# Performance work log

Measured on AMD Instinct MI355X. Metric: run time of the kernel, lower is better.

The kernel has to match this reference:

```python
import jax, jax.numpy as jnp
import numpy as np


def setup_inputs() -> dict:
    key = jax.random.key(0)
    k1, k2, k3 = jax.random.split(key, 3)
    N, Ci, H, W = 16, 64, 224, 224
    Co, K = 128, 3
    x = jax.random.normal(k1, (N, Ci, H, W), dtype=jnp.float32)
    # Kaiming-like scale for conv weight
    conv_weight = jax.random.normal(k2, (Co, Ci, K, K), dtype=jnp.float32) * (1.0 / np.sqrt(Ci * K * K))
    conv_bias = jax.random.normal(k3, (Co,), dtype=jnp.float32) * 0.01
    return {"x": x, "conv_weight": conv_weight, "conv_bias": conv_bias}


def reference(x, conv_weight, conv_bias):
    # conv2d, stride=1, padding=0 (VALID), NCHW / OIHW
    y = jax.lax.conv_general_dilated(
        x, conv_weight,
        window_strides=(1, 1),
        padding="VALID",
        dimension_numbers=("NCHW", "OIHW", "NCHW"),
    ) + conv_bias[None, :, None, None]  # [N, Co, OH, OW]
    # min over output channels (keepdim), then double tanh
    m = jnp.min(y, axis=1, keepdims=True)  # [N, 1, OH, OW]
    return jnp.tanh(jnp.tanh(m))
```

## Files before the change

### kernel.cpp

```cpp
#include <hip/hip_runtime.h>
#include <hip/hip_bf16.h>
#include <math.h>

#define NN   16
#define CI   64
#define HH   224
#define WW   224
#define CO   128
#define OHH  222
#define OWW  222

#define WS_NEED (36*4*64*16)

typedef short  short8  __attribute__((ext_vector_type(8)));
typedef float  f32x16  __attribute__((ext_vector_type(16)));
typedef float  f32x4   __attribute__((ext_vector_type(4)));

__device__ static inline unsigned f2bf_pk(float a, float b) {
  __hip_bfloat162 h = __float22bfloat162_rn(make_float2(a, b));
  return *reinterpret_cast<unsigned*>(&h);
}

__global__ __launch_bounds__(256) void prep_w_kernel(const float* __restrict__ wt,
                                                     unsigned char* __restrict__ ws) {
  int t    = blockIdx.x * 256 + threadIdx.x;
  int lane = t & 63;
  int f    = t >> 6;
  int s    = f >> 2;
  int ct   = f & 3;
  int tap  = s >> 2;
  int cic  = s & 3;
  int kh   = tap / 3, kw = tap % 3;
  int co   = ct * 32 + (lane & 31);
  int k0   = cic * 16 + (lane >> 5) * 8;
  unsigned pk[4];
#pragma unroll
  for (int j = 0; j < 4; ++j) {
    int ci0 = k0 + 2 * j;
    float a = wt[(size_t)co * 576 + (ci0    ) * 9 + kh * 3 + kw];
    float b = wt[(size_t)co * 576 + (ci0 + 1) * 9 + kh * 3 + kw];
    pk[j] = f2bf_pk(a, b);
  }
  ((uint4*)ws)[t] = make_uint4(pk[0], pk[1], pk[2], pk[3]);
}

__global__ __launch_bounds__(512, 4) void conv_min_kernel(
    const float* __restrict__ x, const float* __restrict__ bias,
    const unsigned char* __restrict__ ws, float* __restrict__ out) {
  __shared__ __align__(16) unsigned char smem[10 * 34 * 128];

  int bid = blockIdx.x;
  bid = (bid & 7) * (NN * 28 * 7 / 8) + (bid >> 3);

  int owt  = bid % 7;
  int rest = bid / 7;
  int oht  = rest % 28;
  int n    = rest / 28;
  int ow0  = (owt < 6) ? owt * 32 : 190;
  int oh0  = oht * 8;

  int tid   = threadIdx.x;
  int wv    = tid >> 6;
  int lane  = tid & 63;
  int mg    = wv >> 1;
  int ng    = wv & 1;
  int mrow  = lane & 31;
  int khalf = lane >> 5;

  const short8* wf = (const short8*)ws;
  int bbase = ng * 128 + lane;
  short8 bb[3][2];
#pragma unroll
  for (int ct = 0; ct < 2; ++ct) bb[0][ct] = wf[0 * 256 + ct * 64 + bbase];
#pragma unroll
  for (int ct = 0; ct < 2; ++ct) bb[1][ct] = wf[1 * 256 + ct * 64 + bbase];

  {
    int colm = (tid & 15) * 2;
    int q    = tid >> 4;
    const float* xb = x + (size_t)n * 64 * 50176;
#pragma unroll 1
    for (int r = 0; r < 10; ++r) {
      int rg = oh0 + r; if (rg > 223) rg = 223;
      const float* xr = xb + (size_t)rg * 224;
      {
        int ci = q * 2;
        const float* s0 = xr + (size_t)ci * 50176 + ow0 + colm;
        float2 a2 = *(const float2*)s0;
        float2 b2 = *(const float2*)(s0 + 50176);
        unsigned u0 = f2bf_pk(a2.x, b2.x);
        unsigned u1 = f2bf_pk(a2.y, b2.y);
        int cc = q >> 2, jw = (q & 3) * 4;
        *(unsigned*)(smem + (r * 34 + colm    ) * 128 + (((cc + colm    ) & 7) << 4) + jw) = u0;
        *(unsigned*)(smem + (r * 34 + colm + 1) * 128 + (((cc + colm + 1) & 7) << 4) + jw) = u1;
      }
      if (tid < 64) {
        int cole = 32 + (tid & 1);
        int ppe  = tid >> 1;
        const float* s0 = xr + (size_t)(ppe * 2) * 50176 + ow0 + cole;
        float a = s0[0], b = s0[50176];
        *(unsigned*)(smem + (r * 34 + cole) * 128 + ((((ppe >> 2) + cole) & 7) << 4) + (ppe & 3) * 4) =
            f2bf_pk(a, b);
      }
    }
  }

  f32x16 acc[2][2];
#pragma unroll
  for (int ct = 0; ct < 2; ++ct) {
    float bv = bias[ng * 64 + ct * 32 + mrow];
#pragma unroll
    for (int ohl = 0; ohl < 2; ++ohl)
#pragma unroll
      for (int r = 0; r < 16; ++r) acc[ohl][ct][r] = bv;
  }

  unsigned uu = (mrow + khalf) & 7;
  const unsigned char* Pb = smem + (mg * 2 * 34 + mrow) * 128;
  const unsigned char* P[8];
#pragma unroll
  for (int j = 0; j < 8; ++j) P[j] = Pb + ((uu + j) & 7) * 16;

  __syncthreads();

  short8 aa[2][2];
#pragma unroll
  for (int ohl = 0; ohl < 2; ++ohl)
    aa[0][ohl] = *(const short8*)(P[0] + ((ohl * 34) << 7));

#pragma unroll
  for (int s = 0; s < 36; ++s) {
    if (s + 2 < 36) {
#pragma unroll
      for (int ct = 0; ct < 2; ++ct)
        bb[(s + 2) % 3][ct] = wf[(s + 2) * 256 + ct * 64 + bbase];
    }
    if (s + 1 < 36) {
      const int s1 = s + 1;
      const int kh1 = s1 / 12, kw1 = (s1 / 4) % 3, cic1 = s1 & 3;
      const int j1 = (2 * cic1 + kw1) & 7;
#pragma unroll
      for (int ohl = 0; ohl < 2; ++ohl)
        aa[s1 & 1][ohl] =
            *(const short8*)(P[j1] + ((((ohl + kh1) * 34) + kw1) << 7));
    }
#pragma unroll
    for (int ohl = 0; ohl < 2; ++ohl)
#pragma unroll
      for (int ct = 0; ct < 2; ++ct)
        acc[ohl][ct] = __builtin_amdgcn_mfma_f32_32x32x16_bf16(
            aa[s & 1][ohl], bb[s % 3][ct], acc[ohl][ct], 0, 0, 0);
  }

  __syncthreads();
  float* epi = (float*)smem;
#pragma unroll
  for (int ohl = 0; ohl < 2; ++ohl) {
#pragma unroll
    for (int r = 0; r < 16; ++r) {
      float v = fminf(acc[ohl][0][r], acc[ohl][1][r]);
      v = fminf(v, __shfl_xor(v, 16, 64));
      if ((lane & 16) == 0) {
        int px = (mg * 2 + ohl) * 32 + ((r & 3) + 8 * (r >> 2) + 4 * khalf);
        epi[px * 36 + ng * 16 + (lane & 15)] = v;
      }
    }
  }
  __syncthreads();
  if (tid < 256) {
    int px = tid;
    int oh = oh0 + (px >> 5);
    const f32x4* rowp = (const f32x4*)(epi + px * 36);
    f32x4 m4 = rowp[0];
#pragma unroll
    for (int k = 1; k < 8; ++k) {
      f32x4 t = rowp[k];
      m4[0] = fminf(m4[0], t[0]); m4[1] = fminf(m4[1], t[1]);
      m4[2] = fminf(m4[2], t[2]); m4[3] = fminf(m4[3], t[3]);
    }
    float v = fminf(fminf(m4[0], m4[1]), fminf(m4[2], m4[3]));
    v = tanhf(tanhf(v));
    if (oh < OHH)
      out[(size_t)n * (OHH * OWW) + (size_t)oh * OWW + ow0 + (px & 31)] = v;
  }
}

__global__ __launch_bounds__(128) void fallback_kernel(
    const float* __restrict__ x, const float* __restrict__ wt,
    const float* __restrict__ bias, float* __restrict__ out) {
  __shared__ float patch[64 * 30];
  __shared__ float red[128];
  int pb   = blockIdx.x;
  int owt  = pb % 28;
  int rest = pb / 28;
  int oh   = rest % OHH;
  int n    = rest / OHH;
  int ow0  = owt * 8;
  int tid  = threadIdx.x;
  for (int i = tid; i < 1920; i += 128) {
    int wl = i % 10;
    int rr = (i / 10) % 3;
    int ci = i / 30;
    int wg = ow0 + wl;
    float v = 0.f;
    if (wg < WW) v = x[((size_t)(n * 64 + ci) * HH + (oh + rr)) * WW + wg];
    patch[i] = v;
  }
  __syncthreads();
  int co = tid;
  float a[8];
#pragma unroll
  for (int p = 0; p < 8; ++p) a[p] = bias[co];
  for (int ci = 0; ci < 64; ++ci) {
#pragma unroll
    for (int rr = 0; rr < 3; ++rr)
#pragma unroll
      for (int kw = 0; kw < 3; ++kw) {
        float wvv = wt[(size_t)co * 576 + ci * 9 + rr * 3 + kw];
        const float* pp = &patch[ci * 30 + rr * 10 + kw];
#pragma unroll
        for (int p = 0; p < 8; ++p) a[p] += pp[p] * wvv;
      }
  }
  for (int p = 0; p < 8; ++p) {
    red[tid] = a[p];
    __syncthreads();
    for (int st = 64; st > 0; st >>= 1) {
      if (tid < st) red[tid] = fminf(red[tid], red[tid + st]);
      __syncthreads();
    }
    if (tid == 0 && (ow0 + p) < OWW)
      out[(size_t)n * (OHH * OWW) + (size_t)oh * OWW + ow0 + p] = tanhf(tanhf(red[0]));
    __syncthreads();
  }
}

extern "C" void kernel_launch(void* const* d_in, const int* in_sizes, int n_in,
                              void* d_out, int out_size, void* d_ws, size_t ws_size,
                              hipStream_t stream) {
  const float* x    = (const float*)d_in[0];
  const float* wt   = (const float*)d_in[1];
  const float* bias = (const float*)d_in[2];
  float* out        = (float*)d_out;

  if (ws_size >= WS_NEED) {
    unsigned char* ws = (unsigned char*)d_ws;
    prep_w_kernel<<<36, 256, 0, stream>>>(wt, ws);
    conv_min_kernel<<<NN * 28 * 7, 512, 0, stream>>>(x, bias, ws, out);
  } else {
    fallback_kernel<<<NN * OHH * 28, 128, 0, stream>>>(x, wt, bias, out);
  }
}
```

Baseline: 446.9 us.

## Stage weights through LDS with double-buffered global_load_lds and batch input loads

Weight fragments, which each wave used to load from global memory into registers every step, are now copied chunk by chunk into a double-buffered LDS region using async global_load_lds. The next chunk is prefetched while MFMAs run on the current one, with a barrier after each chunk. The input tile loads are also restructured so that all ten rows of global loads are issued up front before the bf16 conversion and LDS stores, which raises memory-level parallelism. The cost is 32KB more LDS per block, which may reduce occupancy, plus extra barriers inside the main loop.

```diff
diff --git a/kernel.cpp b/kernel.cpp
--- a/kernel.cpp
+++ b/kernel.cpp
@@ -12,6 +12,10 @@
 
 #define WS_NEED (36*4*64*16)
 
+#define A_BYTES (10*34*128)
+#define BCHUNK  16384
+#define NCHUNK  9
+
 typedef short  short8  __attribute__((ext_vector_type(8)));
 typedef float  f32x16  __attribute__((ext_vector_type(16)));
 typedef float  f32x4   __attribute__((ext_vector_type(4)));
@@ -19,6 +23,12 @@
 __device__ static inline unsigned f2bf_pk(float a, float b) {
   __hip_bfloat162 h = __float22bfloat162_rn(make_float2(a, b));
   return *reinterpret_cast<unsigned*>(&h);
+}
+
+__device__ static inline void gload_lds16(const void* g, void* l) {
+  __builtin_amdgcn_global_load_lds(
+      (const __attribute__((address_space(1))) unsigned int*)g,
+      (__attribute__((address_space(3))) unsigned int*)l, 16, 0, 0);
 }
 
 __global__ __launch_bounds__(256) void prep_w_kernel(const float* __restrict__ wt,
@@ -47,7 +57,7 @@
 __global__ __launch_bounds__(512, 4) void conv_min_kernel(
     const float* __restrict__ x, const float* __restrict__ bias,
     const unsigned char* __restrict__ ws, float* __restrict__ out) {
-  __shared__ __align__(16) unsigned char smem[10 * 34 * 128];
+  __shared__ __align__(16) unsigned char smem[A_BYTES + 2 * BCHUNK];
 
   int bid = blockIdx.x;
   bid = (bid & 7) * (NN * 28 * 7 / 8) + (bid >> 3);
@@ -67,41 +77,53 @@
   int mrow  = lane & 31;
   int khalf = lane >> 5;
 
-  const short8* wf = (const short8*)ws;
-  int bbase = ng * 128 + lane;
-  short8 bb[3][2];
-#pragma unroll
-  for (int ct = 0; ct < 2; ++ct) bb[0][ct] = wf[0 * 256 + ct * 64 + bbase];
-#pragma unroll
-  for (int ct = 0; ct < 2; ++ct) bb[1][ct] = wf[1 * 256 + ct * 64 + bbase];
-
   {
+#pragma unroll
+    for (int r = 0; r < 2; ++r)
+      gload_lds16(ws + r * 8192 + (size_t)tid * 16,
+                  smem + A_BYTES + r * 8192 + (size_t)tid * 16);
+
+    const float* xb = x + (size_t)n * 64 * 50176;
     int colm = (tid & 15) * 2;
     int q    = tid >> 4;
-    const float* xb = x + (size_t)n * 64 * 50176;
-#pragma unroll 1
+    int cc   = q >> 2, jw = (q & 3) * 4;
+    int w0off = (((cc + colm    ) & 7) << 4) + jw;
+    int w1off = (((cc + colm + 1) & 7) << 4) + jw;
+    const float* xm = xb + (size_t)(q * 2) * 50176 + ow0 + colm;
+    float2 A2[10], B2[10];
+#pragma unroll
     for (int r = 0; r < 10; ++r) {
       int rg = oh0 + r; if (rg > 223) rg = 223;
-      const float* xr = xb + (size_t)rg * 224;
-      {
-        int ci = q * 2;
-        const float* s0 = xr + (size_t)ci * 50176 + ow0 + colm;
-        float2 a2 = *(const float2*)s0;
-        float2 b2 = *(const float2*)(s0 + 50176);
-        unsigned u0 = f2bf_pk(a2.x, b2.x);
-        unsigned u1 = f2bf_pk(a2.y, b2.y);
-        int cc = q >> 2, jw = (q & 3) * 4;
-        *(unsigned*)(smem + (r * 34 + colm    ) * 128 + (((cc + colm    ) & 7) << 4) + jw) = u0;
-        *(unsigned*)(smem + (r * 34 + colm + 1) * 128 + (((cc + colm + 1) & 7) << 4) + jw) = u1;
-      }
-      if (tid < 64) {
-        int cole = 32 + (tid & 1);
-        int ppe  = tid >> 1;
-        const float* s0 = xr + (size_t)(ppe * 2) * 50176 + ow0 + cole;
-        float a = s0[0], b = s0[50176];
-        *(unsigned*)(smem + (r * 34 + cole) * 128 + ((((ppe >> 2) + cole) & 7) << 4) + (ppe & 3) * 4) =
-            f2bf_pk(a, b);
-      }
+      const float* s0 = xm + (size_t)rg * 224;
+      A2[r] = *(const float2*)s0;
+      B2[r] = *(const float2*)(s0 + 50176);
+    }
+    int cole = 32 + ((tid >> 5) & 1);
+    int ppe  = tid & 31;
+    int re   = tid >> 6;
+    const float* xe = xb + (size_t)(ppe * 2) * 50176 + ow0 + cole;
+    int rg1 = oh0 + re; if (rg1 > 223) rg1 = 223;
+    float ea = xe[(size_t)rg1 * 224];
+    float eb = xe[(size_t)rg1 * 224 + 50176];
+    float ea2 = 0.f, eb2 = 0.f;
+    int re2 = 8 + (tid >> 6);
+    if (tid < 128) {
+      int rg2 = oh0 + re2; if (rg2 > 223) rg2 = 223;
+      ea2 = xe[(size_t)rg2 * 224];
+      eb2 = xe[(size_t)rg2 * 224 + 50176];
+    }
+#pragma unroll
+    for (int r = 0; r < 10; ++r) {
+      unsigned u0 = f2bf_pk(A2[r].x, B2[r].x);
+      unsigned u1 = f2bf_pk(A2[r].y, B2[r].y);
+      *(unsigned*)(smem + (r * 34 + colm    ) * 128 + w0off) = u0;
+      *(unsigned*)(smem + (r * 34 + colm + 1) * 128 + w1off) = u1;
+    }
+    {
+      int eoff = ((((ppe >> 2) + cole) & 7) << 4) + (ppe & 3) * 4;
+      *(unsigned*)(smem + (re * 34 + cole) * 128 + eoff) = f2bf_pk(ea, eb);
+      if (tid < 128)
+        *(unsigned*)(smem + (re2 * 34 + cole) * 128 + eoff) = f2bf_pk(ea2, eb2);
     }
   }
 
@@ -121,35 +143,58 @@
 #pragma unroll
   for (int j = 0; j < 8; ++j) P[j] = Pb + ((uu + j) & 7) * 16;
 
-  __syncthreads();
-
-  short8 aa[2][2];
+  const unsigned char* Bw = smem + A_BYTES + ng * 2048 + lane * 16;
+
+  __syncthreads();
+
+  short8 aa[2][2], bb[2][2];
 #pragma unroll
   for (int ohl = 0; ohl < 2; ++ohl)
     aa[0][ohl] = *(const short8*)(P[0] + ((ohl * 34) << 7));
-
-#pragma unroll
-  for (int s = 0; s < 36; ++s) {
-    if (s + 2 < 36) {
+#pragma unroll
+  for (int ct = 0; ct < 2; ++ct)
+    bb[0][ct] = *(const short8*)(Bw + 0 * 4096 + ct * 1024);
+
+#pragma unroll
+  for (int ch = 0; ch < NCHUNK; ++ch) {
+    const int p = ch & 1;
+    if (ch + 1 < NCHUNK) {
+#pragma unroll
+      for (int r = 0; r < 2; ++r)
+        gload_lds16(ws + (ch + 1) * BCHUNK + r * 8192 + (size_t)tid * 16,
+                    smem + A_BYTES + (p ^ 1) * BCHUNK + r * 8192 + (size_t)tid * 16);
+    }
+#pragma unroll
+    for (int si = 0; si < 4; ++si) {
+      const int s = ch * 4 + si;
+      if (si < 3) {
+#pragma unroll
+        for (int ct = 0; ct < 2; ++ct)
+          bb[(si + 1) & 1][ct] =
+              *(const short8*)(Bw + p * BCHUNK + (si + 1) * 4096 + ct * 1024);
+      }
+      if (s + 1 < 36) {
+        const int s1 = s + 1;
+        const int kh1 = s1 / 12, kw1 = (s1 / 4) % 3, cic1 = s1 & 3;
+        const int j1 = (2 * cic1 + kw1) & 7;
+#pragma unroll
+        for (int ohl = 0; ohl < 2; ++ohl)
+          aa[s1 & 1][ohl] =
+              *(const short8*)(P[j1] + ((((ohl + kh1) * 34) + kw1) << 7));
+      }
+#pragma unroll
+      for (int ohl = 0; ohl < 2; ++ohl)
+#pragma unroll
+        for (int ct = 0; ct < 2; ++ct)
+          acc[ohl][ct] = __builtin_amdgcn_mfma_f32_32x32x16_bf16(
+              aa[s & 1][ohl], bb[si & 1][ct], acc[ohl][ct], 0, 0, 0);
+    }
+    if (ch + 1 < NCHUNK) {
+      __syncthreads();
 #pragma unroll
       for (int ct = 0; ct < 2; ++ct)
-        bb[(s + 2) % 3][ct] = wf[(s + 2) * 256 + ct * 64 + bbase];
-    }
-    if (s + 1 < 36) {
-      const int s1 = s + 1;
-      const int kh1 = s1 / 12, kw1 = (s1 / 4) % 3, cic1 = s1 & 3;
-      const int j1 = (2 * cic1 + kw1) & 7;
-#pragma unroll
-      for (int ohl = 0; ohl < 2; ++ohl)
-        aa[s1 & 1][ohl] =
-            *(const short8*)(P[j1] + ((((ohl + kh1) * 34) + kw1) << 7));
-    }
-#pragma unroll
-    for (int ohl = 0; ohl < 2; ++ohl)
-#pragma unroll
-      for (int ct = 0; ct < 2; ++ct)
-        acc[ohl][ct] = __builtin_amdgcn_mfma_f32_32x32x16_bf16(
-            aa[s & 1][ohl], bb[s % 3][ct], acc[ohl][ct], 0, 0, 0);
+        bb[0][ct] = *(const short8*)(Bw + (p ^ 1) * BCHUNK + 0 * 4096 + ct * 1024);
+    }
   }
 
   __syncthreads();
```

Result: faster. 365.7 us (-18.2%).
